# Optimization experiments

Hardware: AMD Instinct MI355X
Metric: run time of the kernel (lower is better)

The kernel has to match this reference:

```python
import jax, jax.numpy as jnp
import numpy as np

N, E = 10000, 160000
IN_DIM, HID, HEADS, EDGE_DIM = 1024, 1024, 8, 4
HEAD_DIM = HID // HEADS  # 128
NEG_SLOPE = 0.2
EPS = 1e-16  # PyG softmax denominator epsilon


def _lin(key, fan_in, fan_out, bias=True):
    kw, kb = jax.random.split(key)
    s = 1.0 / np.sqrt(fan_in)
    W = jax.random.uniform(kw, (fan_in, fan_out), minval=-s, maxval=s, dtype=jnp.float32)
    if not bias:
        return W
    b = jax.random.uniform(kb, (fan_out,), minval=-s, maxval=s, dtype=jnp.float32)
    return W, b


def setup_inputs() -> dict:
    key = jax.random.key(0)
    ks = jax.random.split(key, 24)
    x = jax.random.normal(ks[0], (N, IN_DIM), dtype=jnp.float32)
    edge_index = jax.random.randint(ks[1], (2, E), 0, N, dtype=jnp.int64)
    edge_attr = jax.random.normal(ks[2], (E, EDGE_DIM), dtype=jnp.float32)

    W_in, b_in = _lin(ks[3], IN_DIM, HID)

    def gat_params(k):
        k0, k1, k2, k3, k4 = jax.random.split(k, 5)
        Wl, bl = _lin(k0, HID, HID)
        Wr, br = _lin(k1, HID, HID)
        We = _lin(k2, EDGE_DIM, HID, bias=False)
        att = jax.random.normal(k3, (HEADS, HEAD_DIM), dtype=jnp.float32) / np.sqrt(HEAD_DIM)
        b = jnp.zeros((HID,), dtype=jnp.float32)
        return Wl, bl, Wr, br, We, att, b

    g1 = gat_params(ks[4])
    g2 = gat_params(ks[5])
    m1_W, m1_b = _lin(ks[6], HID, 512)
    m2_W, m2_b = _lin(ks[7], 512, 128)
    m3_W, m3_b = _lin(ks[8], 128, 1)

    names1 = ['g1_Wl', 'g1_bl', 'g1_Wr', 'g1_br', 'g1_We', 'g1_att', 'g1_b']
    names2 = ['g2_Wl', 'g2_bl', 'g2_Wr', 'g2_br', 'g2_We', 'g2_att', 'g2_b']
    out = {'x': x, 'edge_index': edge_index, 'edge_attr': edge_attr,
           'W_in': W_in, 'b_in': b_in,
           'm1_W': m1_W, 'm1_b': m1_b, 'm2_W': m2_W, 'm2_b': m2_b,
           'm3_W': m3_W, 'm3_b': m3_b}
    out.update(dict(zip(names1, g1)))
    out.update(dict(zip(names2, g2)))
    return out


def gatv2_layer(x, src, dst, edge_attr, Wl, bl, Wr, br, We, att, bias):
    # x: [N, HID]; returns [N, HID] (heads concatenated)
    xl = (x @ Wl + bl).reshape(-1, HEADS, HEAD_DIM)  # source transform
    xr = (x @ Wr + br).reshape(-1, HEADS, HEAD_DIM)  # target transform
    e = (edge_attr @ We).reshape(-1, HEADS, HEAD_DIM)
    m = jax.nn.leaky_relu(xl[src] + xr[dst] + e, NEG_SLOPE)  # [E, H, D]
    logits = jnp.einsum('ehd,hd->eh', m, att)  # [E, H]
    lmax = jax.ops.segment_max(logits, dst, num_segments=N)
    lmax = jnp.where(jnp.isfinite(lmax), lmax, 0.0)
    ex = jnp.exp(logits - lmax[dst])
    denom = jax.ops.segment_sum(ex, dst, num_segments=N)
    alpha = ex / (denom[dst] + EPS)  # [E, H]
    out = jax.ops.segment_sum(xl[src] * alpha[..., None], dst, num_segments=N)
    return out.reshape(-1, HID) + bias


def reference(x, edge_index, edge_attr, W_in, b_in,
              g1_Wl, g1_bl, g1_Wr, g1_br, g1_We, g1_att, g1_b,
              g2_Wl, g2_bl, g2_Wr, g2_br, g2_We, g2_att, g2_b,
              m1_W, m1_b, m2_W, m2_b, m3_W, m3_b):
    src, dst = edge_index[0], edge_index[1]
    h = jax.nn.elu(x @ W_in + b_in)
    h = jax.nn.elu(gatv2_layer(h, src, dst, edge_attr, g1_Wl, g1_bl, g1_Wr, g1_br, g1_We, g1_att, g1_b))
    h = jax.nn.elu(gatv2_layer(h, src, dst, edge_attr, g2_Wl, g2_bl, g2_Wr, g2_br, g2_We, g2_att, g2_b))
    h = jax.nn.relu(h @ m1_W + m1_b)
    h = jax.nn.relu(h @ m2_W + m2_b)
    return jax.nn.sigmoid(h @ m3_W + m3_b)  # [N, 1]
```

## Files before the change

### kernel.cpp

```cpp
#include <hip/hip_runtime.h>
#include <math.h>

constexpr int HID = 1024;
constexpr float NEG_SLOPE = 0.2f;
constexpr float EPSV = 1e-16f;

typedef __bf16 bf16x8 __attribute__((ext_vector_type(8)));
typedef float f32x4 __attribute__((ext_vector_type(4)));
typedef float f32x2 __attribute__((ext_vector_type(2)));
typedef unsigned short us8 __attribute__((ext_vector_type(8)));
typedef unsigned short us4 __attribute__((ext_vector_type(4)));
typedef unsigned short ushort_t;

#define AS1 __attribute__((address_space(1)))
#define AS3 __attribute__((address_space(3)))

__device__ __forceinline__ float4 ld4(const float* p){ return *reinterpret_cast<const float4*>(p); }
__device__ __forceinline__ float b2f(ushort_t u){ return __uint_as_float(((unsigned)u) << 16); }
__device__ __forceinline__ ushort_t f2b(float f){
  unsigned u = __float_as_uint(f);
  return (ushort_t)((u + 0x7FFFu + ((u >> 16) & 1u)) >> 16);
}
__device__ __forceinline__ float rfl(float x){
  return __uint_as_float(__builtin_amdgcn_readfirstlane(__float_as_uint(x)));
}
__device__ __forceinline__ f32x2 up2(unsigned u){
  f32x2 r;
  r[0] = __uint_as_float(u << 16);
  r[1] = __uint_as_float(u & 0xffff0000u);
  return r;
}
__device__ __forceinline__ f32x2 lrelu2(f32x2 v){
  return __builtin_elementwise_max(v, v * NEG_SLOPE);
}

struct TP5 { const float* src[5]; ushort_t* dst[5]; };
__global__ __launch_bounds__(256) void transpose_f2b_5(TP5 p){
  const int z = blockIdx.z;
  const float* W = p.src[z];
  ushort_t* WT = p.dst[z];
  __shared__ float tile[32][33];
  const int tx = threadIdx.x & 31, ty = threadIdx.x >> 5;
  const int n0 = blockIdx.x * 32, k0 = blockIdx.y * 32;
  #pragma unroll
  for (int r = 0; r < 32; r += 8)
    tile[ty + r][tx] = W[(size_t)(k0 + ty + r) * 1024 + n0 + tx];
  __syncthreads();
  #pragma unroll
  for (int r = 0; r < 32; r += 8)
    WT[(size_t)(n0 + ty + r) * 1024 + k0 + tx] = f2b(tile[tx][ty + r]);
}

__global__ __launch_bounds__(256) void transpose_f2b(const float* __restrict__ W, ushort_t* __restrict__ WT,
                                                     int K, int N){
  __shared__ float tile[32][33];
  const int tx = threadIdx.x & 31, ty = threadIdx.x >> 5;
  const int n0 = blockIdx.x * 32, k0 = blockIdx.y * 32;
  #pragma unroll
  for (int r = 0; r < 32; r += 8)
    tile[ty + r][tx] = W[(size_t)(k0 + ty + r) * N + n0 + tx];
  __syncthreads();
  #pragma unroll
  for (int r = 0; r < 32; r += 8)
    WT[(size_t)(n0 + ty + r) * K + k0 + tx] = f2b(tile[tx][ty + r]);
}

struct BC4 { const float* s[4]; };
__global__ void concat_bias(BC4 p, float* __restrict__ dst){
  const int i = blockIdx.x * blockDim.x + threadIdx.x;
  dst[i] = p.s[i >> 10][i & 1023];
}

__global__ void convert_f2b(const float* __restrict__ in, ushort_t* __restrict__ out, size_t n){
  size_t i = ((size_t)blockIdx.x * blockDim.x + threadIdx.x) * 4;
  const size_t stride = (size_t)gridDim.x * blockDim.x * 4;
  for (; i < n; i += stride){
    const float4 v = ld4(in + i);
    us4 o = {f2b(v.x), f2b(v.y), f2b(v.z), f2b(v.w)};
    *reinterpret_cast<us4*>(out + i) = o;
  }
}

template<int ACT, int OUTB>
__global__ __launch_bounds__(512, 4) void gemm_mfma(
    const ushort_t* __restrict__ A, const ushort_t* __restrict__ BT,
    const float* __restrict__ bias, float* __restrict__ Cf, ushort_t* __restrict__ Cb,
    int M, int K, int N)
{
  __shared__ __align__(16) char smem[65536];
  ushort_t* Asl = (ushort_t*)smem;
  ushort_t* Bsl = (ushort_t*)(smem + 32768);
  const int tid = threadIdx.x;
  const int lane = tid & 63, wave = tid >> 6;
  const int wr = (wave >> 1) * 32;
  const int wc = (wave & 1) * 64;

  const int nwg = gridDim.x * gridDim.y;
  int wg = blockIdx.y * gridDim.x + blockIdx.x;
  {
    const int q = nwg >> 3, r = nwg & 7;
    const int xcd = wg & 7, lo = wg >> 3;
    wg = (xcd < r ? xcd * (q + 1) : r * (q + 1) + (xcd - r) * q) + lo;
  }
  const int bm = (wg / gridDim.x) * 128, bn = (wg % gridDim.x) * 128;

  const int mrow = lane & 15;
  const int r0 = (lane >> 4) * 4;

  f32x4 acc[2][4];
  #pragma unroll
  for (int i = 0; i < 2; ++i)
    #pragma unroll
    for (int j = 0; j < 4; ++j)
      acc[i][j] = (f32x4){0.f, 0.f, 0.f, 0.f};

  const int srow = tid >> 3;
  const int ssl = (((lane & 7) ^ (lane >> 3))) * 8;
  const int ldst = wave * 512 + lane * 8;

  auto stage = [&](int buf, int k0){
    #pragma unroll
    for (int q = 0; q < 2; ++q){
      const int row = q * 64 + srow;
      int arow = bm + row; if (arow > M - 1) arow = M - 1;
      __builtin_amdgcn_global_load_lds(
        (const AS1 unsigned int*)(A + (size_t)arow * K + k0 + ssl),
        (AS3 unsigned int*)(Asl + buf * 8192 + q * 4096 + ldst), 16, 0, 0);
      __builtin_amdgcn_global_load_lds(
        (const AS1 unsigned int*)(BT + (size_t)(bn + row) * K + k0 + ssl),
        (AS3 unsigned int*)(Bsl + buf * 8192 + q * 4096 + ldst), 16, 0, 0);
    }
  };

  const int kslice = (lane >> 4);
  auto compute = [&](int buf){
    #pragma unroll
    for (int ks = 0; ks < 2; ++ks){
      bf16x8 af[2], bfr[4];
      #pragma unroll
      for (int i = 0; i < 2; ++i){
        const int row = wr + i * 16 + mrow;
        const int sl = (ks * 4 + kslice) ^ (row & 7);
        af[i] = *reinterpret_cast<const bf16x8*>(&Asl[buf * 8192 + row * 64 + sl * 8]);
      }
      #pragma unroll
      for (int j = 0; j < 4; ++j){
        const int row = wc + j * 16 + mrow;
        const int sl = (ks * 4 + kslice) ^ (row & 7);
        bfr[j] = *reinterpret_cast<const bf16x8*>(&Bsl[buf * 8192 + row * 64 + sl * 8]);
      }
      #pragma unroll
      for (int i = 0; i < 2; ++i)
        #pragma unroll
        for (int j = 0; j < 4; ++j)
          acc[i][j] = __builtin_amdgcn_mfma_f32_16x16x32_bf16(af[i], bfr[j], acc[i][j], 0, 0, 0);
    }
  };

  stage(0, 0);
  asm volatile("s_waitcnt vmcnt(0)" ::: "memory");
  __builtin_amdgcn_s_barrier();

  const int NT = K >> 6;
  int cur = 0;
  for (int t = 0; t < NT; ++t){
    if (t + 1 < NT) stage(cur ^ 1, (t + 1) << 6);
    compute(cur);
    asm volatile("s_waitcnt vmcnt(0)" ::: "memory");
    __builtin_amdgcn_s_barrier();
    cur ^= 1;
  }

  float* ldsF = (float*)smem;
  const int wbase = wave * 2048;
  #pragma unroll
  for (int i = 0; i < 2; ++i)
    #pragma unroll
    for (int j = 0; j < 4; ++j)
      #pragma unroll
      for (int r = 0; r < 4; ++r)
        ldsF[wbase + (i * 16 + r0 + r) * 64 + j * 16 + mrow] = acc[i][j][r];
  asm volatile("s_waitcnt lgkmcnt(0)" ::: "memory");

  const int lrow = lane >> 3, lcol = (lane & 7) * 8;
  #pragma unroll
  for (int i2 = 0; i2 < 4; ++i2){
    const int row = bm + wr + i2 * 8 + lrow;
    const int col = bn + wc + lcol;
    if (row < M){
      const f32x4 lo = *reinterpret_cast<const f32x4*>(&ldsF[wbase + (i2 * 8 + lrow) * 64 + lcol]);
      const f32x4 hi = *reinterpret_cast<const f32x4*>(&ldsF[wbase + (i2 * 8 + lrow) * 64 + lcol + 4]);
      const float4 b0 = ld4(bias + col), b1 = ld4(bias + col + 4);
      float v[8] = {lo[0] + b0.x, lo[1] + b0.y, lo[2] + b0.z, lo[3] + b0.w,
                    hi[0] + b1.x, hi[1] + b1.y, hi[2] + b1.z, hi[3] + b1.w};
      #pragma unroll
      for (int u = 0; u < 8; ++u){
        float t2 = v[u];
        if (ACT == 1) t2 = fmaxf(t2, 0.f);
        else if (ACT == 2) t2 = (t2 > 0.f) ? t2 : expm1f(t2);
        v[u] = t2;
      }
      if (OUTB){
        us8 ov;
        #pragma unroll
        for (int u = 0; u < 8; ++u) ov[u] = f2b(v[u]);
        *reinterpret_cast<us8*>(Cb + (size_t)row * N + col) = ov;
      } else {
        *reinterpret_cast<float4*>(Cf + (size_t)row * N + col)     = make_float4(v[0], v[1], v[2], v[3]);
        *reinterpret_cast<float4*>(Cf + (size_t)row * N + col + 4) = make_float4(v[4], v[5], v[6], v[7]);
      }
    }
  }
}

__global__ void count_deg(const int* __restrict__ dst, int* __restrict__ deg, int E){
  int e = blockIdx.x * blockDim.x + threadIdx.x;
  if (e < E) atomicAdd(&deg[dst[e]], 1);
}

__global__ __launch_bounds__(1024) void scan_offsets(const int* __restrict__ deg, int* __restrict__ offs, int n){
  __shared__ int ws[16];
  const int tid = threadIdx.x, lane = tid & 63, wid = tid >> 6;
  int running = 0;
  for (int base = 0; base < n; base += 1024){
    const int i = base + tid;
    const int v = (i < n) ? deg[i] : 0;
    int x = v;
    #pragma unroll
    for (int s = 1; s < 64; s <<= 1){
      int u = __shfl_up(x, s, 64);
      if (lane >= s) x += u;
    }
    if (lane == 63) ws[wid] = x;
    __syncthreads();
    if (tid < 16){
      int p = ws[tid];
      #pragma unroll
      for (int s = 1; s < 16; s <<= 1){
        int u = __shfl_up(p, s, 64);
        if (tid >= s) p += u;
      }
      ws[tid] = p;
    }
    __syncthreads();
    const int wpre = (wid > 0) ? ws[wid - 1] : 0;
    if (i < n) offs[i] = running + wpre + x - v;
    running += ws[15];
    __syncthreads();
  }
  if (tid == 0) offs[n] = running;
}

__global__ void fill_csr(const int* __restrict__ src, const int* __restrict__ dst,
                         const float* __restrict__ edge_attr,
                         const int* __restrict__ offs, int* __restrict__ cursor,
                         int* __restrict__ csr_src, float* __restrict__ csr_ea, int E){
  int e = blockIdx.x * blockDim.x + threadIdx.x;
  if (e < E){
    int d = dst[e];
    int pos = offs[d] + atomicAdd(&cursor[d], 1);
    csr_src[pos] = src[e];
    *reinterpret_cast<float4*>(csr_ea + (size_t)pos * 4) = ld4(edge_attr + (size_t)e * 4);
  }
}

__global__ __launch_bounds__(128) void fused_gat(
    const int* __restrict__ offs, const int* __restrict__ csr_src, const float* __restrict__ csr_ea,
    const float* __restrict__ We, const float* __restrict__ att,
    const ushort_t* __restrict__ xlr, const float* __restrict__ bias,
    ushort_t* __restrict__ out, int N)
{
  const int n = blockIdx.x;
  const int t = threadIdx.x;
  const int d0 = t * 8;

  f32x2 W0[4], W1[4], W2[4], W3[4], AT[4];
  #pragma unroll
  for (int q = 0; q < 4; ++q){
    W0[q] = *reinterpret_cast<const f32x2*>(We + d0 + 2*q);
    W1[q] = *reinterpret_cast<const f32x2*>(We + 1024 + d0 + 2*q);
    W2[q] = *reinterpret_cast<const f32x2*>(We + 2048 + d0 + 2*q);
    W3[q] = *reinterpret_cast<const f32x2*>(We + 3072 + d0 + 2*q);
    AT[q] = *reinterpret_cast<const f32x2*>(att + d0 + 2*q);
  }
  f32x2 xr[4];
  {
    const uint4 xu = *reinterpret_cast<const uint4*>(xlr + (size_t)n * 2048 + 1024 + d0);
    xr[0] = up2(xu.x); xr[1] = up2(xu.y); xr[2] = up2(xu.z); xr[3] = up2(xu.w);
  }

  const int o0 = __builtin_amdgcn_readfirstlane(offs[n]);
  const int o1 = __builtin_amdgcn_readfirstlane(offs[n + 1]);

  f32x2 acc[4];
  #pragma unroll
  for (int q = 0; q < 4; ++q) acc[q] = (f32x2){0.f, 0.f};
  float lsum = 0.f, mcur = -1e30f;

  uint4 xa = {0u,0u,0u,0u}, xb = {0u,0u,0u,0u};
  float eA0=0.f,eA1=0.f,eA2=0.f,eA3=0.f, eB0=0.f,eB1=0.f,eB2=0.f,eB3=0.f;

  auto ldedge = [&](int idx, uint4& xv, float& e0, float& e1, float& e2, float& e3){
    const int s = __builtin_amdgcn_readfirstlane(csr_src[idx]);
    xv = *reinterpret_cast<const uint4*>(xlr + (size_t)s * 2048 + d0);
    const float4 e = ld4(csr_ea + (size_t)idx * 4);
    e0 = rfl(e.x); e1 = rfl(e.y); e2 = rfl(e.z); e3 = rfl(e.w);
  };

  if (o0 < o1)     ldedge(o0,     xa, eA0,eA1,eA2,eA3);
  if (o0 + 1 < o1) ldedge(o0 + 1, xb, eB0,eB1,eB2,eB3);

  int i = o0;
  while (i < o1){
    const uint4 ca = xa; const float a0=eA0,a1=eA1,a2=eA2,a3=eA3;
    const uint4 cb = xb; const float b0=eB0,b1=eB1,b2=eB2,b3=eB3;
    const bool pair = (i + 1 < o1);
    const int ni = i + 2;
    if (ni < o1)     ldedge(ni,     xa, eA0,eA1,eA2,eA3);
    if (ni + 1 < o1) ldedge(ni + 1, xb, eB0,eB1,eB2,eB3);

    f32x2 xav[4] = {up2(ca.x), up2(ca.y), up2(ca.z), up2(ca.w)};
    f32x2 xbv[4] = {up2(cb.x), up2(cb.y), up2(cb.z), up2(cb.w)};

    f32x2 za2 = {0.f,0.f}, zb2 = {0.f,0.f};
    #pragma unroll
    for (int q = 0; q < 4; ++q){
      f32x2 ma = xav[q] + xr[q];
      ma += W0[q]*a0; ma += W1[q]*a1; ma += W2[q]*a2; ma += W3[q]*a3;
      ma = lrelu2(ma);
      za2 += ma * AT[q];
      f32x2 mb = xbv[q] + xr[q];
      mb += W0[q]*b0; mb += W1[q]*b1; mb += W2[q]*b2; mb += W3[q]*b3;
      mb = lrelu2(mb);
      zb2 += mb * AT[q];
    }
    float zA = za2[0] + za2[1];
    float zB = zb2[0] + zb2[1];
    #pragma unroll
    for (int sh = 1; sh <= 8; sh <<= 1){
      zA += __shfl_xor(zA, sh, 64);
      zB += __shfl_xor(zB, sh, 64);
    }

    if (pair){
      const float mn = fmaxf(fmaxf(mcur, zA), zB);
      const float sc = __expf(mcur - mn);
      const float pA = __expf(zA - mn);
      const float pB = __expf(zB - mn);
      lsum = lsum * sc + pA + pB;
      #pragma unroll
      for (int q = 0; q < 4; ++q)
        acc[q] = acc[q] * sc + xav[q] * pA + xbv[q] * pB;
      mcur = mn;
    } else {
      const float mn = fmaxf(mcur, zA);
      const float sc = __expf(mcur - mn);
      const float pA = __expf(zA - mn);
      lsum = lsum * sc + pA;
      #pragma unroll
      for (int q = 0; q < 4; ++q)
        acc[q] = acc[q] * sc + xav[q] * pA;
      mcur = mn;
    }
    i = ni;
  }

  const float r = 1.f / (lsum + EPSV);
  const float4 bv0 = ld4(bias + d0);
  const float4 bv1 = ld4(bias + d0 + 4);
  float o_[8] = {acc[0][0]*r + bv0.x, acc[0][1]*r + bv0.y, acc[1][0]*r + bv0.z, acc[1][1]*r + bv0.w,
                 acc[2][0]*r + bv1.x, acc[2][1]*r + bv1.y, acc[3][0]*r + bv1.z, acc[3][1]*r + bv1.w};
  us8 ov;
  #pragma unroll
  for (int j = 0; j < 8; ++j){
    float v = o_[j];
    v = (v > 0.f) ? v : expm1f(v);
    ov[j] = f2b(v);
  }
  *reinterpret_cast<us8*>(out + (size_t)n * HID + d0) = ov;
}

__global__ __launch_bounds__(256) void mlp_final(const float* __restrict__ h, const float* __restrict__ w,
                                                 const float* __restrict__ b, float* __restrict__ out, int M)
{
  const int row = (int)((blockIdx.x * (size_t)blockDim.x + threadIdx.x) >> 6);
  const int lane = threadIdx.x & 63;
  if (row >= M) return;
  const float2 v  = *reinterpret_cast<const float2*>(&h[(size_t)row * 128 + lane * 2]);
  const float2 ww = *reinterpret_cast<const float2*>(&w[lane * 2]);
  float s = v.x * ww.x + v.y * ww.y;
  #pragma unroll
  for (int m = 1; m <= 32; m <<= 1) s += __shfl_xor(s, m, 64);
  if (lane == 0) out[row] = 1.f / (1.f + expf(-(s + b[0])));
}

extern "C" void kernel_launch(void* const* d_in, const int* in_sizes, int n_in,
                              void* d_out, int out_size, void* d_ws, size_t ws_size,
                              hipStream_t stream)
{
  const float* x        = (const float*)d_in[0];
  const int*   ei       = (const int*)d_in[1];
  const float* edge_attr= (const float*)d_in[2];
  const float* W_in     = (const float*)d_in[3];
  const float* b_in     = (const float*)d_in[4];
  const float* m1_W     = (const float*)d_in[5];
  const float* m1_b     = (const float*)d_in[6];
  const float* m2_W     = (const float*)d_in[7];
  const float* m2_b     = (const float*)d_in[8];
  const float* m3_W     = (const float*)d_in[9];
  const float* m3_b     = (const float*)d_in[10];
  const float* g_Wl[2]  = {(const float*)d_in[11], (const float*)d_in[18]};
  const float* g_bl[2]  = {(const float*)d_in[12], (const float*)d_in[19]};
  const float* g_Wr[2]  = {(const float*)d_in[13], (const float*)d_in[20]};
  const float* g_br[2]  = {(const float*)d_in[14], (const float*)d_in[21]};
  const float* g_We[2]  = {(const float*)d_in[15], (const float*)d_in[22]};
  const float* g_att[2] = {(const float*)d_in[16], (const float*)d_in[23]};
  const float* g_b[2]   = {(const float*)d_in[17], (const float*)d_in[24]};

  const int Nn = in_sizes[0] / 1024;
  const int E  = in_sizes[1] / 2;
  const int* srcv = ei;
  const int* dstv = ei + E;
  float* out = (float*)d_out;

  char* wsp = (char*)d_ws;
  size_t off = 0;
  auto alloc = [&](size_t bytes)->char* {
    char* p = wsp + off;
    off = (off + bytes + 255) & ~(size_t)255;
    return p;
  };
  ushort_t* hbf  = (ushort_t*)alloc((size_t)Nn * HID * 2);
  ushort_t* ubuf = (ushort_t*)alloc((size_t)Nn * HID * 2);
  ushort_t* xlr  = (ushort_t*)alloc((size_t)Nn * 2048 * 2);
  float*    m2f  = (float*)   alloc((size_t)Nn * 128 * 4);
  ushort_t* WinT = (ushort_t*)alloc((size_t)1024 * 1024 * 2);
  ushort_t* Wlr0 = (ushort_t*)alloc((size_t)2048 * 1024 * 2);
  ushort_t* Wlr1 = (ushort_t*)alloc((size_t)2048 * 1024 * 2);
  ushort_t* m1T  = (ushort_t*)alloc((size_t)512 * 1024 * 2);
  ushort_t* m2T  = (ushort_t*)alloc((size_t)128 * 512 * 2);
  float*  biasc  = (float*)   alloc((size_t)2048 * 2 * 4);
  int* deg    = (int*)alloc((size_t)Nn * 2 * 4);
  int* cursor = deg + Nn;
  int* offs   = (int*)alloc((size_t)(Nn + 1) * 4);
  int* csr_src= (int*)alloc((size_t)E * 4);
  float* csr_ea = (float*)alloc((size_t)E * 4 * 4);
  ushort_t* Wlr[2]  = {Wlr0, Wlr1};
  float*    blr[2]  = {biasc, biasc + 2048};

  TP5 tp;
  tp.src[0] = W_in;    tp.dst[0] = WinT;
  tp.src[1] = g_Wl[0]; tp.dst[1] = Wlr0;
  tp.src[2] = g_Wr[0]; tp.dst[2] = Wlr0 + 1024*1024;
  tp.src[3] = g_Wl[1]; tp.dst[3] = Wlr1;
  tp.src[4] = g_Wr[1]; tp.dst[4] = Wlr1 + 1024*1024;
  transpose_f2b_5<<<dim3(32, 32, 5), 256, 0, stream>>>(tp);
  transpose_f2b<<<dim3(16, 32), 256, 0, stream>>>(m1_W, m1T, 1024, 512);
  transpose_f2b<<<dim3(4, 16), 256, 0, stream>>>(m2_W, m2T, 512, 128);
  convert_f2b<<<2048, 256, 0, stream>>>(x, ubuf, (size_t)Nn * HID);
  BC4 bc; bc.s[0] = g_bl[0]; bc.s[1] = g_br[0]; bc.s[2] = g_bl[1]; bc.s[3] = g_br[1];
  concat_bias<<<16, 256, 0, stream>>>(bc, biasc);

  hipMemsetAsync(deg, 0, (size_t)Nn * 2 * 4, stream);
  count_deg<<<(E + 255)/256, 256, 0, stream>>>(dstv, deg, E);
  scan_offsets<<<1, 1024, 0, stream>>>(deg, offs, Nn);
  fill_csr<<<(E + 255)/256, 256, 0, stream>>>(srcv, dstv, edge_attr, offs, cursor, csr_src, csr_ea, E);

  const int MB = (Nn + 127) / 128;
  gemm_mfma<2, 1><<<dim3(8, MB), 512, 0, stream>>>(ubuf, WinT, b_in, nullptr, hbf, Nn, 1024, 1024);

  for (int L = 0; L < 2; ++L){
    gemm_mfma<0, 1><<<dim3(16, MB), 512, 0, stream>>>(hbf, Wlr[L], blr[L], nullptr, xlr, Nn, 1024, 2048);
    fused_gat<<<Nn, 128, 0, stream>>>(offs, csr_src, csr_ea, g_We[L], g_att[L], xlr, g_b[L], hbf, Nn);
  }

  gemm_mfma<1, 1><<<dim3(4, MB), 512, 0, stream>>>(hbf, m1T, m1_b, nullptr, ubuf, Nn, 1024, 512);
  gemm_mfma<1, 0><<<dim3(1, MB), 512, 0, stream>>>(ubuf, m2T, m2_b, m2f, nullptr, Nn, 512, 128);
  mlp_final<<<((size_t)Nn * 64 + 255)/256, 256, 0, stream>>>(m2f, m3_W, m3_b, out, Nn);
}
```

Measured before the change: 345.4 us.

## Add 256x256 tile MFMA GEMM for GAT Wl/Wr projections

Adds a new bf16 MFMA GEMM kernel with 256x256 output tiles, a double-buffered LDS pipeline loaded via global_load_lds, XCD-aware workgroup remapping, and an LDS-staged epilogue. It is used for the two 10000x1024x2048 GAT projection GEMMs in place of the 128-row tile kernel. The aim is more data reuse per loaded tile and fewer workgroups. In exchange it uses 128KB of LDS per block, which limits occupancy, and the grid is small (8x40), which may underfill the CUs.

```diff
diff --git a/kernel.cpp b/kernel.cpp
--- a/kernel.cpp
+++ b/kernel.cpp
@@ -210,6 +210,141 @@
         *reinterpret_cast<float4*>(Cf + (size_t)row * N + col + 4) = make_float4(v[4], v[5], v[6], v[7]);
       }
     }
+  }
+}
+
+template<int ACT, int OUTB>
+__global__ __launch_bounds__(512, 2) void gemm_mfma256(
+    const ushort_t* __restrict__ A, const ushort_t* __restrict__ BT,
+    const float* __restrict__ bias, float* __restrict__ Cf, ushort_t* __restrict__ Cb,
+    int M, int K, int N)
+{
+  __shared__ __align__(16) char smem[131072];
+  ushort_t* Asl = (ushort_t*)smem;
+  ushort_t* Bsl = (ushort_t*)(smem + 65536);
+  const int tid = threadIdx.x;
+  const int lane = tid & 63, wave = tid >> 6;
+  const int wr = (wave >> 2) * 128;
+  const int wc = (wave & 3) * 64;
+
+  const int nwg = gridDim.x * gridDim.y;
+  int wg = blockIdx.y * gridDim.x + blockIdx.x;
+  {
+    const int q = nwg >> 3, r = nwg & 7;
+    const int xcd = wg & 7, lo = wg >> 3;
+    wg = (xcd < r ? xcd * (q + 1) : r * (q + 1) + (xcd - r) * q) + lo;
+  }
+  const int bm = (wg / gridDim.x) * 256, bn = (wg % gridDim.x) * 256;
+
+  const int mrow = lane & 15;
+  const int r0 = (lane >> 4) * 4;
+
+  f32x4 acc[8][4];
+  #pragma unroll
+  for (int i = 0; i < 8; ++i)
+    #pragma unroll
+    for (int j = 0; j < 4; ++j)
+      acc[i][j] = (f32x4){0.f, 0.f, 0.f, 0.f};
+
+  const int ssl = ((lane & 7) ^ (lane >> 3)) * 8;
+  const int lsub = wave * 512 + lane * 8;
+
+  auto stage = [&](int buf, int k0){
+    #pragma unroll
+    for (int q = 0; q < 4; ++q){
+      const int row = q * 64 + wave * 8 + (lane >> 3);
+      int arow = bm + row; if (arow > M - 1) arow = M - 1;
+      __builtin_amdgcn_global_load_lds(
+        (const AS1 unsigned int*)(A + (size_t)arow * K + k0 + ssl),
+        (AS3 unsigned int*)(Asl + buf * 16384 + q * 4096 + lsub), 16, 0, 0);
+      __builtin_amdgcn_global_load_lds(
+        (const AS1 unsigned int*)(BT + (size_t)(bn + row) * K + k0 + ssl),
+        (AS3 unsigned int*)(Bsl + buf * 16384 + q * 4096 + lsub), 16, 0, 0);
+    }
+  };
+
+  const int kslice = lane >> 4;
+  auto compute = [&](int buf){
+    #pragma unroll
+    for (int ks = 0; ks < 2; ++ks){
+      bf16x8 af[8], bfr[4];
+      #pragma unroll
+      for (int i = 0; i < 8; ++i){
+        const int row = wr + i * 16 + mrow;
+        const int sl = (ks * 4 + kslice) ^ (row & 7);
+        af[i] = *reinterpret_cast<const bf16x8*>(&Asl[buf * 16384 + row * 64 + sl * 8]);
+      }
+      #pragma unroll
+      for (int j = 0; j < 4; ++j){
+        const int row = wc + j * 16 + mrow;
+        const int sl = (ks * 4 + kslice) ^ (row & 7);
+        bfr[j] = *reinterpret_cast<const bf16x8*>(&Bsl[buf * 16384 + row * 64 + sl * 8]);
+      }
+      #pragma unroll
+      for (int i = 0; i < 8; ++i)
+        #pragma unroll
+        for (int j = 0; j < 4; ++j)
+          acc[i][j] = __builtin_amdgcn_mfma_f32_16x16x32_bf16(af[i], bfr[j], acc[i][j], 0, 0, 0);
+    }
+  };
+
+  stage(0, 0);
+  asm volatile("s_waitcnt vmcnt(0)" ::: "memory");
+  __builtin_amdgcn_s_barrier();
+
+  const int NT = K >> 6;
+  int cur = 0;
+  for (int t = 0; t < NT; ++t){
+    if (t + 1 < NT) stage(cur ^ 1, (t + 1) << 6);
+    compute(cur);
+    asm volatile("s_waitcnt vmcnt(0)" ::: "memory");
+    __builtin_amdgcn_s_barrier();
+    cur ^= 1;
+  }
+
+  float* ldsF = (float*)smem;
+  const int wbase = wave * 4096;
+  const int lrow = lane >> 3, lcol = (lane & 7) * 8;
+  #pragma unroll
+  for (int half = 0; half < 2; ++half){
+    #pragma unroll
+    for (int i = 0; i < 4; ++i)
+      #pragma unroll
+      for (int j = 0; j < 4; ++j)
+        #pragma unroll
+        for (int r = 0; r < 4; ++r)
+          ldsF[wbase + (i * 16 + r0 + r) * 64 + j * 16 + mrow] = acc[half * 4 + i][j][r];
+    asm volatile("s_waitcnt lgkmcnt(0)" ::: "memory");
+    #pragma unroll
+    for (int i3 = 0; i3 < 8; ++i3){
+      const int rl = i3 * 8 + lrow;
+      const int row = bm + wr + half * 64 + rl;
+      const int col = bn + wc + lcol;
+      if (row < M){
+        const f32x4 lo = *reinterpret_cast<const f32x4*>(&ldsF[wbase + rl * 64 + lcol]);
+        const f32x4 hi = *reinterpret_cast<const f32x4*>(&ldsF[wbase + rl * 64 + lcol + 4]);
+        const float4 b0 = ld4(bias + col), b1 = ld4(bias + col + 4);
+        float v[8] = {lo[0] + b0.x, lo[1] + b0.y, lo[2] + b0.z, lo[3] + b0.w,
+                      hi[0] + b1.x, hi[1] + b1.y, hi[2] + b1.z, hi[3] + b1.w};
+        #pragma unroll
+        for (int u = 0; u < 8; ++u){
+          float t2 = v[u];
+          if (ACT == 1) t2 = fmaxf(t2, 0.f);
+          else if (ACT == 2) t2 = (t2 > 0.f) ? t2 : expm1f(t2);
+          v[u] = t2;
+        }
+        if (OUTB){
+          us8 ov;
+          #pragma unroll
+          for (int u = 0; u < 8; ++u) ov[u] = f2b(v[u]);
+          *reinterpret_cast<us8*>(Cb + (size_t)row * N + col) = ov;
+        } else {
+          *reinterpret_cast<float4*>(Cf + (size_t)row * N + col)     = make_float4(v[0], v[1], v[2], v[3]);
+          *reinterpret_cast<float4*>(Cf + (size_t)row * N + col + 4) = make_float4(v[4], v[5], v[6], v[7]);
+        }
+      }
+    }
+    asm volatile("s_waitcnt lgkmcnt(0)" ::: "memory");
   }
 }
 
@@ -467,10 +602,11 @@
   fill_csr<<<(E + 255)/256, 256, 0, stream>>>(srcv, dstv, edge_attr, offs, cursor, csr_src, csr_ea, E);
 
   const int MB = (Nn + 127) / 128;
+  const int MB2 = (Nn + 255) / 256;
   gemm_mfma<2, 1><<<dim3(8, MB), 512, 0, stream>>>(ubuf, WinT, b_in, nullptr, hbf, Nn, 1024, 1024);
 
   for (int L = 0; L < 2; ++L){
-    gemm_mfma<0, 1><<<dim3(16, MB), 512, 0, stream>>>(hbf, Wlr[L], blr[L], nullptr, xlr, Nn, 1024, 2048);
+    gemm_mfma256<0, 1><<<dim3(8, MB2), 512, 0, stream>>>(hbf, Wlr[L], blr[L], nullptr, xlr, Nn, 1024, 2048);
     fused_gat<<<Nn, 128, 0, stream>>>(offs, csr_src, csr_ea, g_We[L], g_att[L], xlr, g_b[L], hbf, Nn);
   }
 
```

New measurement: 371.1 us. 7.5% more time.
